# Kernel tuning notes

Measured on AMD Instinct MI355X. Metric: run time of the kernel, lower is better.

The kernel has to match this reference:

```python
import jax, jax.numpy as jnp
import numpy as np
import math

D, H = 128, 8
B, LC, LQ = 8, 512, 64


def pos_signal(channels, length):
    # tensor2tensor timing signal, returned as [C, L]
    pos = jnp.arange(length, dtype=jnp.float32)
    nts = channels // 2
    inc = math.log(1.0e4) / (nts - 1)
    inv = jnp.exp(jnp.arange(nts, dtype=jnp.float32) * -inc)
    st = pos[:, None] * inv[None, :]                      # [L, nts]
    sig = jnp.concatenate([jnp.sin(st), jnp.cos(st)], 1)  # [L, C]
    return sig.T


def mask_logits(t, m):
    return t * m + (1.0 - m) * -1e30


def ln_c(x, g, b):  # LayerNorm over channel dim of [B, D, L]
    mu = jnp.mean(x, axis=1, keepdims=True)
    var = jnp.mean((x - mu) ** 2, axis=1, keepdims=True)
    return (x - mu) / jnp.sqrt(var + 1e-5) * g[None, :, None] + b[None, :, None]


def conv1x1(x, w, b=None):  # x [B, I, L], w [O, I]
    y = jnp.einsum('oi,bil->bol', w, x)
    return y if b is None else y + b[None, :, None]


def dw_sep_conv(x, dw, pw, pwb):  # depthwise (k, no bias) -> pointwise (bias) -> relu
    k = dw.shape[-1]
    y = jax.lax.conv_general_dilated(x, dw[:, None, :], (1,), [(k // 2, k // 2)],
        dimension_numbers=('NCH', 'OIH', 'NCH'), feature_group_count=x.shape[1])
    return jax.nn.relu(conv1x1(y, pw, pwb))


def self_attention(x, mem_w, q_w, mask, n_head):  # x [B, D, L]
    b, d, L = x.shape
    dh = d // n_head
    mem = jnp.einsum('oi,bil->blo', mem_w, x)  # [B, L, 2D]
    q = jnp.einsum('oi,bil->blo', q_w, x)      # [B, L, D]
    def heads(t):
        return t.reshape(b, L, n_head, dh).transpose(0, 2, 1, 3)  # [B, H, L, dh]
    Qh = heads(q) * dh ** -0.5
    K = heads(mem[..., :d])
    V = heads(mem[..., d:])
    logits = jnp.einsum('bhqe,bhke->bhqk', Qh, K)
    logits = mask_logits(logits, mask[:, None, None, :])
    w = jax.nn.softmax(logits, axis=-1)
    o = jnp.einsum('bhqk,bhke->bhqe', w, V)
    return o.transpose(0, 2, 1, 3).reshape(b, L, d).transpose(0, 2, 1)


def encoder_block(x, mask, p, n_head):
    out = x + pos_signal(x.shape[1], x.shape[2])[None]
    n_conv = p['dw'].shape[0]
    for i in range(n_conv):
        res = out
        out = ln_c(out, p['lnc_g'][i], p['lnc_b'][i])
        out = dw_sep_conv(out, p['dw'][i], p['pw'][i], p['pw_b'][i]) + res
    res = out
    out = ln_c(out, p['ln1_g'], p['ln1_b'])
    out = self_attention(out, p['mem_w'], p['q_w'], mask, n_head) + res
    res = out
    out = ln_c(out, p['ln2_g'], p['ln2_b'])
    out = jax.nn.relu(conv1x1(out, p['ffn1_w'], p['ffn1_b']))
    out = conv1x1(out, p['ffn2_w'], p['ffn2_b'])
    return out + res


def cq_attention(Ce, Qe, cmask, qmask, w4C, w4Q, w4mlu, cq_b):
    Cx = Ce.transpose(0, 2, 1)   # [B, Lc, 2D]
    Qx = Qe.transpose(0, 2, 1)   # [B, Lq, 2D]
    s0 = jnp.einsum('bld,d->bl', Cx, w4C)[:, :, None]
    s1 = jnp.einsum('bqd,d->bq', Qx, w4Q)[:, None, :]
    s2 = jnp.einsum('bld,bqd->blq', Cx * w4mlu[None, None, :], Qx)
    S = s0 + s1 + s2 + cq_b
    S1 = jax.nn.softmax(mask_logits(S, qmask[:, None, :]), axis=2)
    S2 = jax.nn.softmax(mask_logits(S, cmask[:, :, None]), axis=1)
    A = jnp.einsum('blq,bqd->bld', S1, Qx)
    Bt = jnp.einsum('blq,bmq,bmd->bld', S1, S2, Cx)  # (S1 @ S2^T) @ C
    out = jnp.concatenate([Cx, A, Cx * A, Cx * Bt], axis=2)
    return out.transpose(0, 2, 1)  # [B, 8D, Lc]


def _forward(C, Q, maskC, maskQ, e_dw, e_pw, e_pw_b, e_lnc_g, e_lnc_b, e_mem_w, e_q_w,
             e_ffn1_w, e_ffn1_b, e_ffn2_w, e_ffn2_b, e_ln1_g, e_ln1_b, e_ln2_g, e_ln2_b,
             w4C, w4Q, w4mlu, cq_b, resizer_w,
             m_dw, m_pw, m_pw_b, m_lnc_g, m_lnc_b, m_mem_w, m_q_w,
             m_ffn1_w, m_ffn1_b, m_ffn2_w, m_ffn2_b, m_ln1_g, m_ln1_b, m_ln2_g, m_ln2_b):
    ep = dict(dw=e_dw, pw=e_pw, pw_b=e_pw_b, lnc_g=e_lnc_g, lnc_b=e_lnc_b,
              mem_w=e_mem_w, q_w=e_q_w, ffn1_w=e_ffn1_w, ffn1_b=e_ffn1_b,
              ffn2_w=e_ffn2_w, ffn2_b=e_ffn2_b, ln1_g=e_ln1_g, ln1_b=e_ln1_b,
              ln2_g=e_ln2_g, ln2_b=e_ln2_b)
    mp = dict(dw=m_dw, pw=m_pw, pw_b=m_pw_b, lnc_g=m_lnc_g, lnc_b=m_lnc_b,
              mem_w=m_mem_w, q_w=m_q_w, ffn1_w=m_ffn1_w, ffn1_b=m_ffn1_b,
              ffn2_w=m_ffn2_w, ffn2_b=m_ffn2_b, ln1_g=m_ln1_g, ln1_b=m_ln1_b,
              ln2_g=m_ln2_g, ln2_b=m_ln2_b)
    Ce = encoder_block(C, maskC, ep, H)
    Qe = encoder_block(Q, maskQ, ep, H)
    Ce = jnp.concatenate([Ce, C], axis=1)  # encode_fusion -> [B, 2D, Lc]
    Qe = jnp.concatenate([Qe, Q], axis=1)
    X = cq_attention(Ce, Qe, maskC, maskQ, w4C, w4Q, w4mlu, cq_b)
    X = jnp.concatenate([X, Ce], axis=1)   # match_fusion -> [B, 10D, Lc]
    M0 = conv1x1(X, resizer_w)             # [B, D, Lc]

    def run(m):
        def step(carry, p):
            return encoder_block(carry, maskC, p, H), None
        m, _ = jax.lax.scan(step, m, mp)
        return m

    M1 = run(M0)
    M2 = run(M1)
    M3 = run(M2)
    return M1, M2, M3


def setup_inputs() -> dict:
    key = jax.random.key(0)
    ks = iter(jax.random.split(key, 48))
    def rn(shape, scale):
        return jax.random.normal(next(ks), shape, dtype=jnp.float32) * scale
    s1 = 1.0 / math.sqrt(D)
    s2 = 1.0 / math.sqrt(2 * D)
    f32 = jnp.float32
    return dict(
        C=rn((B, D, LC), 1.0), Q=rn((B, D, LQ), 1.0),
        maskC=jnp.ones((B, LC), f32), maskQ=jnp.ones((B, LQ), f32),
        e_dw=rn((4, D, 7), 1.0 / math.sqrt(7)), e_pw=rn((4, D, D), s1),
        e_pw_b=jnp.zeros((4, D), f32), e_lnc_g=jnp.ones((4, D), f32), e_lnc_b=jnp.zeros((4, D), f32),
        e_mem_w=rn((2 * D, D), s1), e_q_w=rn((D, D), s1),
        e_ffn1_w=rn((D, D), s1), e_ffn1_b=jnp.zeros((D,), f32),
        e_ffn2_w=rn((D, D), s1), e_ffn2_b=jnp.zeros((D,), f32),
        e_ln1_g=jnp.ones((D,), f32), e_ln1_b=jnp.zeros((D,), f32),
        e_ln2_g=jnp.ones((D,), f32), e_ln2_b=jnp.zeros((D,), f32),
        w4C=rn((2 * D,), s2), w4Q=rn((2 * D,), s2), w4mlu=rn((2 * D,), s2),
        cq_b=jnp.zeros((1,), f32),
        resizer_w=rn((D, 10 * D), 1.0 / math.sqrt(10 * D)),
        m_dw=rn((7, 2, D, 5), 1.0 / math.sqrt(5)), m_pw=rn((7, 2, D, D), s1),
        m_pw_b=jnp.zeros((7, 2, D), f32), m_lnc_g=jnp.ones((7, 2, D), f32), m_lnc_b=jnp.zeros((7, 2, D), f32),
        m_mem_w=rn((7, 2 * D, D), s1), m_q_w=rn((7, D, D), s1),
        m_ffn1_w=rn((7, D, D), s1), m_ffn1_b=jnp.zeros((7, D), f32),
        m_ffn2_w=rn((7, D, D), s1), m_ffn2_b=jnp.zeros((7, D), f32),
        m_ln1_g=jnp.ones((7, D), f32), m_ln1_b=jnp.zeros((7, D), f32),
        m_ln2_g=jnp.ones((7, D), f32), m_ln2_b=jnp.zeros((7, D), f32),
    )


def reference(C, Q, maskC, maskQ, e_dw, e_pw, e_pw_b, e_lnc_g, e_lnc_b, e_mem_w, e_q_w,
              e_ffn1_w, e_ffn1_b, e_ffn2_w, e_ffn2_b, e_ln1_g, e_ln1_b, e_ln2_g, e_ln2_b,
              w4C, w4Q, w4mlu, cq_b, resizer_w,
              m_dw, m_pw, m_pw_b, m_lnc_g, m_lnc_b, m_mem_w, m_q_w,
              m_ffn1_w, m_ffn1_b, m_ffn2_w, m_ffn2_b, m_ln1_g, m_ln1_b, m_ln2_g, m_ln2_b):
    return _forward(C, Q, maskC, maskQ, e_dw, e_pw, e_pw_b, e_lnc_g, e_lnc_b, e_mem_w, e_q_w,
                    e_ffn1_w, e_ffn1_b, e_ffn2_w, e_ffn2_b, e_ln1_g, e_ln1_b, e_ln2_g, e_ln2_b,
                    w4C, w4Q, w4mlu, cq_b, resizer_w,
                    m_dw, m_pw, m_pw_b, m_lnc_g, m_lnc_b, m_mem_w, m_q_w,
                    m_ffn1_w, m_ffn1_b, m_ffn2_w, m_ffn2_b, m_ln1_g, m_ln1_b, m_ln2_g, m_ln2_b)
```

## Files before the change

kernel.cpp:

```cpp
#include <hip/hip_runtime.h>
#include <math.h>

#define D_  128
#define B_  8
#define H_  8
#define LC_ 512
#define LQ_ 64

typedef float f32x4 __attribute__((ext_vector_type(4)));
typedef short bf16x8 __attribute__((ext_vector_type(8)));
typedef short short4v __attribute__((ext_vector_type(4)));
typedef unsigned short ushortT;

__device__ inline short bfr(float x) {
  unsigned u = __float_as_uint(x);
  u += 0x7fff + ((u >> 16) & 1);
  return (short)(u >> 16);
}
__device__ inline float bfi(ushortT u) {
  return __uint_as_float(((unsigned)u) << 16);
}

__device__ inline bf16x8 mk8(short4v lo, short4v hi) {
  bf16x8 r;
  r[0] = lo[0]; r[1] = lo[1]; r[2] = lo[2]; r[3] = lo[3];
  r[4] = hi[0]; r[5] = hi[1]; r[6] = hi[2]; r[7] = hi[3];
  return r;
}

__device__ inline bf16x8 ldA(const ushortT* row, int koff) {
  short4v lo = *(const short4v*)(row + koff);
  short4v hi = *(const short4v*)(row + koff + 16);
  return mk8(lo, hi);
}
__device__ inline bf16x8 ldB2(const ushortT* plo, const ushortT* phi) {
  short4v lo = *(const short4v*)plo;
  short4v hi = *(const short4v*)phi;
  return mk8(lo, hi);
}

__global__ void k_prep(const float* a0, const float* a1, const float* a2,
                       const float* a3, const float* a4, const float* a5,
                       const float* a6, const float* a7, const float* a8,
                       const float* a9, const float* a10, ushortT* dst) {
  int i = blockIdx.x * 256 + threadIdx.x;
  if (i >= 1114112) return;
  const float* s; int lo;
  if      (i <   65536) { s = a0;  lo = i; }
  else if (i <   98304) { s = a1;  lo = i - 65536; }
  else if (i <  114688) { s = a2;  lo = i - 98304; }
  else if (i <  131072) { s = a3;  lo = i - 114688; }
  else if (i <  147456) { s = a4;  lo = i - 131072; }
  else if (i <  311296) { s = a5;  lo = i - 147456; }
  else if (i <  540672) { s = a6;  lo = i - 311296; }
  else if (i <  770048) { s = a7;  lo = i - 540672; }
  else if (i <  884736) { s = a8;  lo = i - 770048; }
  else if (i <  999424) { s = a9;  lo = i - 884736; }
  else                  { s = a10; lo = i - 999424; }
  dst[i] = (ushortT)bfr(s[lo]);
}

template <int KK, int ADDPOS>
__global__ __launch_bounds__(256) void k_fusedconv(
    const float* __restrict__ x, float* __restrict__ yout,
    const float* __restrict__ dw1, const ushortT* __restrict__ pw1,
    const float* __restrict__ pb1, const float* __restrict__ g1,
    const float* __restrict__ be1,
    const float* __restrict__ dw2, const ushortT* __restrict__ pw2,
    const float* __restrict__ pb2, const float* __restrict__ g2w,
    const float* __restrict__ be2, int L) {
  const int HALO = KK / 2;
  const int W1 = 32 + 2 * HALO;
  __shared__ __align__(16) float raw[128 * 40];
  __shared__ __align__(16) ushortT l1o[128 * 36];
  __shared__ __align__(16) ushortT xbf1[32 * 32 * 4];
  __shared__ float mu1[40], rs1[40], mu2[32], rs2[32], ps[160], psq[160];
  ushortT* xbf2 = (ushortT*)raw;
  int l0 = blockIdx.x * 16;
  int o0 = blockIdx.y * 64;
  int b = blockIdx.z;
  int tid = threadIdx.x;
  for (int idx = tid; idx < 128 * W1; idx += 256) {
    int d = idx / W1, c = idx - d * W1;
    int gl = l0 - 8 - HALO + c;
    float v = 0.f;
    if (gl >= 0 && gl < L) {
      v = x[((size_t)b * 128 + d) * L + gl];
      if (ADDPOS) {
        int j = d & 63;
        float arg = (float)gl * expf(-(float)j * 0.14619588f);
        v += (d < 64) ? sinf(arg) : cosf(arg);
      }
    }
    raw[d * 40 + c] = v;
  }
  __syncthreads();
  if (tid < 4 * W1) {
    int c = tid % W1, hh = tid / W1;
    float s = 0.f, s2 = 0.f;
    for (int d = hh * 32; d < hh * 32 + 32; d++) {
      float v = raw[d * 40 + c];
      s += v; s2 += v * v;
    }
    ps[tid] = s; psq[tid] = s2;
  }
  __syncthreads();
  if (tid < W1) {
    float s = ps[tid] + ps[tid + W1] + ps[tid + 2 * W1] + ps[tid + 3 * W1];
    float s2 = psq[tid] + psq[tid + W1] + psq[tid + 2 * W1] + psq[tid + 3 * W1];
    float mu = s * (1.f / 128.f);
    float var = fmaxf(s2 * (1.f / 128.f) - mu * mu, 0.f);
    mu1[tid] = mu; rs1[tid] = rsqrtf(var + 1e-5f);
  }
  __syncthreads();
  {
    int cc0 = tid & 31, dbase = tid >> 5;
#pragma unroll
    for (int kq = 0; kq < 4; kq++) {
      short4v pk;
#pragma unroll
      for (int e = 0; e < 4; e++) {
        int d = dbase * 16 + kq * 4 + e;
        float gg = g1[d], bb = be1[d];
        const float* wr = dw1 + d * KK;
        float acc = 0.f;
#pragma unroll
        for (int t = 0; t < KK; t++) {
          int ci = cc0 + t;
          int gl = l0 - 8 - HALO + ci;
          float lv = 0.f;
          if (gl >= 0 && gl < L)
            lv = (raw[d * 40 + ci] - mu1[ci]) * rs1[ci] * gg + bb;
          acc += wr[t] * lv;
        }
        pk[e] = bfr(acc);
      }
      *(short4v*)&xbf1[(((dbase * 4 + kq) * 32) + cc0) * 4] = pk;
    }
  }
  __syncthreads();
  int w = tid >> 6, lane = tid & 63, g2 = lane >> 4, r = lane & 15;
  {
    f32x4 acc[2][2];
#pragma unroll
    for (int i = 0; i < 2; i++)
#pragma unroll
      for (int nt = 0; nt < 2; nt++) acc[i][nt] = (f32x4){0.f, 0.f, 0.f, 0.f};
#pragma unroll
    for (int i = 0; i < 2; i++) {
      const ushortT* arow = pw1 + (size_t)((2 * w + i) * 16 + r) * 128;
#pragma unroll
      for (int kk = 0; kk < 4; kk++) {
        bf16x8 a = ldA(arow, kk * 32 + g2 * 4);
#pragma unroll
        for (int nt = 0; nt < 2; nt++) {
          bf16x8 bb = ldB2(&xbf1[(((kk * 8 + g2) * 32) + nt * 16 + r) * 4],
                           &xbf1[(((kk * 8 + 4 + g2) * 32) + nt * 16 + r) * 4]);
          acc[i][nt] = __builtin_amdgcn_mfma_f32_16x16x32_bf16(a, bb, acc[i][nt], 0, 0, 0);
        }
      }
    }
#pragma unroll
    for (int i = 0; i < 2; i++)
#pragma unroll
      for (int nt = 0; nt < 2; nt++)
#pragma unroll
        for (int p = 0; p < 4; p++) {
          int o = (2 * w + i) * 16 + g2 * 4 + p;
          int c1 = nt * 16 + r;
          int gl = l0 - 8 + c1;
          float val = 0.f;
          if (gl >= 0 && gl < L)
            val = fmaxf(acc[i][nt][p] + pb1[o], 0.f) + raw[o * 40 + c1 + HALO];
          l1o[o * 36 + c1] = (ushortT)bfr(val);
        }
  }
  __syncthreads();
  if (tid < 128) {
    int c = tid & 31, hh = tid >> 5;
    float s = 0.f, s2 = 0.f;
    for (int d = hh * 32; d < hh * 32 + 32; d++) {
      float v = bfi(l1o[d * 36 + c]);
      s += v; s2 += v * v;
    }
    ps[tid] = s; psq[tid] = s2;
  }
  __syncthreads();
  if (tid < 32) {
    float s = ps[tid] + ps[tid + 32] + ps[tid + 64] + ps[tid + 96];
    float s2 = psq[tid] + psq[tid + 32] + psq[tid + 64] + psq[tid + 96];
    float mu = s * (1.f / 128.f);
    float var = fmaxf(s2 * (1.f / 128.f) - mu * mu, 0.f);
    mu2[tid] = mu; rs2[tid] = rsqrtf(var + 1e-5f);
  }
  __syncthreads();
  {
    int cc2 = tid & 15, db2 = tid >> 4;
#pragma unroll
    for (int kq = 0; kq < 2; kq++) {
      short4v pk;
#pragma unroll
      for (int e = 0; e < 4; e++) {
        int d = db2 * 8 + kq * 4 + e;
        float gg = g2w[d], bb = be2[d];
        const float* wr = dw2 + d * KK;
        float acc = 0.f;
#pragma unroll
        for (int t = 0; t < KK; t++) {
          int c1 = cc2 + 8 + t - HALO;
          int gl = l0 + cc2 + t - HALO;
          float lv = 0.f;
          if (gl >= 0 && gl < L)
            lv = (bfi(l1o[d * 36 + c1]) - mu2[c1]) * rs2[c1] * gg + bb;
          acc += wr[t] * lv;
        }
        pk[e] = bfr(acc);
      }
      *(short4v*)&xbf2[(((db2 * 2 + kq) * 16) + cc2) * 4] = pk;
    }
  }
  __syncthreads();
  {
    f32x4 a2 = {0.f, 0.f, 0.f, 0.f};
    const ushortT* arow = pw2 + (size_t)(o0 + 16 * w + r) * 128;
#pragma unroll
    for (int kk = 0; kk < 4; kk++) {
      bf16x8 a = ldA(arow, kk * 32 + g2 * 4);
      bf16x8 bb = ldB2(&xbf2[(((kk * 8 + g2) * 16) + r) * 4],
                       &xbf2[(((kk * 8 + 4 + g2) * 16) + r) * 4]);
      a2 = __builtin_amdgcn_mfma_f32_16x16x32_bf16(a, bb, a2, 0, 0, 0);
    }
#pragma unroll
    for (int p = 0; p < 4; p++) {
      int o = o0 + 16 * w + g2 * 4 + p;
      yout[((size_t)b * 128 + o) * L + l0 + r] =
          fmaxf(a2[p] + pb2[o], 0.f) + bfi(l1o[o * 36 + 8 + r]);
    }
  }
}

template <int KK, int ADDPOS>
__global__ __launch_bounds__(512) void k_convproj(
    const float* __restrict__ x, float* __restrict__ yout,
    const float* __restrict__ dw1, const ushortT* __restrict__ pw1,
    const float* __restrict__ pb1, const float* __restrict__ g1,
    const float* __restrict__ be1,
    const float* __restrict__ dw2, const ushortT* __restrict__ pw2,
    const float* __restrict__ pb2, const float* __restrict__ g2w,
    const float* __restrict__ be2,
    const ushortT* __restrict__ memw, const ushortT* __restrict__ qw,
    const float* __restrict__ g3, const float* __restrict__ be3,
    float* __restrict__ mkv, float* __restrict__ qp, int L) {
  const int HALO = KK / 2;
  const int W1 = 32 + 2 * HALO;
  __shared__ __align__(16) float raw[128 * 40];
  __shared__ __align__(16) ushortT l1o[128 * 36];
  __shared__ __align__(16) ushortT xbf1[32 * 32 * 4];
  __shared__ __align__(16) ushortT c2o[128 * 16];
  __shared__ float mu1[40], rs1[40], mu2[32], rs2[32], mu3[16], rs3[16];
  __shared__ float ps[512], psq[512];
  ushortT* xbf2 = (ushortT*)raw;
  ushortT* xbf3 = (ushortT*)(raw + 4096);
  int l0 = blockIdx.x * 16;
  int b = blockIdx.z;
  int tid = threadIdx.x;
  for (int idx = tid; idx < 128 * W1; idx += 512) {
    int d = idx / W1, c = idx - d * W1;
    int gl = l0 - 8 - HALO + c;
    float v = 0.f;
    if (gl >= 0 && gl < L) {
      v = x[((size_t)b * 128 + d) * L + gl];
      if (ADDPOS) {
        int j = d & 63;
        float arg = (float)gl * expf(-(float)j * 0.14619588f);
        v += (d < 64) ? sinf(arg) : cosf(arg);
      }
    }
    raw[d * 40 + c] = v;
  }
  __syncthreads();
  if (tid < 4 * W1) {
    int c = tid % W1, hh = tid / W1;
    float s = 0.f, s2 = 0.f;
    for (int d = hh * 32; d < hh * 32 + 32; d++) {
      float v = raw[d * 40 + c];
      s += v; s2 += v * v;
    }
    ps[tid] = s; psq[tid] = s2;
  }
  __syncthreads();
  if (tid < W1) {
    float s = ps[tid] + ps[tid + W1] + ps[tid + 2 * W1] + ps[tid + 3 * W1];
    float s2 = psq[tid] + psq[tid + W1] + psq[tid + 2 * W1] + psq[tid + 3 * W1];
    float mu = s * (1.f / 128.f);
    float var = fmaxf(s2 * (1.f / 128.f) - mu * mu, 0.f);
    mu1[tid] = mu; rs1[tid] = rsqrtf(var + 1e-5f);
  }
  __syncthreads();
  {
    int cc0 = tid & 31, dbase = tid >> 5;
#pragma unroll
    for (int kq = 0; kq < 2; kq++) {
      short4v pk;
#pragma unroll
      for (int e = 0; e < 4; e++) {
        int d = dbase * 8 + kq * 4 + e;
        float gg = g1[d], bb = be1[d];
        const float* wr = dw1 + d * KK;
        float acc = 0.f;
#pragma unroll
        for (int t = 0; t < KK; t++) {
          int ci = cc0 + t;
          int gl = l0 - 8 - HALO + ci;
          float lv = 0.f;
          if (gl >= 0 && gl < L)
            lv = (raw[d * 40 + ci] - mu1[ci]) * rs1[ci] * gg + bb;
          acc += wr[t] * lv;
        }
        pk[e] = bfr(acc);
      }
      *(short4v*)&xbf1[(((dbase * 2 + kq) * 32) + cc0) * 4] = pk;
    }
  }
  __syncthreads();
  int w = tid >> 6, lane = tid & 63, g2 = lane >> 4, r = lane & 15;
  {
    f32x4 acc[2];
    acc[0] = (f32x4){0.f, 0.f, 0.f, 0.f};
    acc[1] = (f32x4){0.f, 0.f, 0.f, 0.f};
    const ushortT* arow = pw1 + (size_t)(w * 16 + r) * 128;
#pragma unroll
    for (int kk = 0; kk < 4; kk++) {
      bf16x8 a = ldA(arow, kk * 32 + g2 * 4);
#pragma unroll
      for (int nt = 0; nt < 2; nt++) {
        bf16x8 bb = ldB2(&xbf1[(((kk * 8 + g2) * 32) + nt * 16 + r) * 4],
                         &xbf1[(((kk * 8 + 4 + g2) * 32) + nt * 16 + r) * 4]);
        acc[nt] = __builtin_amdgcn_mfma_f32_16x16x32_bf16(a, bb, acc[nt], 0, 0, 0);
      }
    }
#pragma unroll
    for (int nt = 0; nt < 2; nt++)
#pragma unroll
      for (int p = 0; p < 4; p++) {
        int o = w * 16 + g2 * 4 + p;
        int c1 = nt * 16 + r;
        int gl = l0 - 8 + c1;
        float val = 0.f;
        if (gl >= 0 && gl < L)
          val = fmaxf(acc[nt][p] + pb1[o], 0.f) + raw[o * 40 + c1 + HALO];
        l1o[o * 36 + c1] = (ushortT)bfr(val);
      }
  }
  __syncthreads();
  if (tid < 128) {
    int c = tid & 31, hh = tid >> 5;
    float s = 0.f, s2 = 0.f;
    for (int d = hh * 32; d < hh * 32 + 32; d++) {
      float v = bfi(l1o[d * 36 + c]);
      s += v; s2 += v * v;
    }
    ps[tid] = s; psq[tid] = s2;
  }
  __syncthreads();
  if (tid < 32) {
    float s = ps[tid] + ps[tid + 32] + ps[tid + 64] + ps[tid + 96];
    float s2 = psq[tid] + psq[tid + 32] + psq[tid + 64] + psq[tid + 96];
    float mu = s * (1.f / 128.f);
    float var = fmaxf(s2 * (1.f / 128.f) - mu * mu, 0.f);
    mu2[tid] = mu; rs2[tid] = rsqrtf(var + 1e-5f);
  }
  __syncthreads();
  {
    int cc2 = tid & 15, db2 = tid >> 4;
    short4v pk;
#pragma unroll
    for (int e = 0; e < 4; e++) {
      int d = db2 * 4 + e;
      float gg = g2w[d], bb = be2[d];
      const float* wr = dw2 + d * KK;
      float acc = 0.f;
#pragma unroll
      for (int t = 0; t < KK; t++) {
        int c1 = cc2 + 8 + t - HALO;
        int gl = l0 + cc2 + t - HALO;
        float lv = 0.f;
        if (gl >= 0 && gl < L)
          lv = (bfi(l1o[d * 36 + c1]) - mu2[c1]) * rs2[c1] * gg + bb;
        acc += wr[t] * lv;
      }
      pk[e] = bfr(acc);
    }
    *(short4v*)&xbf2[((db2 * 16) + cc2) * 4] = pk;
  }
  __syncthreads();
  {
    f32x4 a2 = {0.f, 0.f, 0.f, 0.f};
    const ushortT* arow = pw2 + (size_t)(w * 16 + r) * 128;
#pragma unroll
    for (int kk = 0; kk < 4; kk++) {
      bf16x8 a = ldA(arow, kk * 32 + g2 * 4);
      bf16x8 bb = ldB2(&xbf2[(((kk * 8 + g2) * 16) + r) * 4],
                       &xbf2[(((kk * 8 + 4 + g2) * 16) + r) * 4]);
      a2 = __builtin_amdgcn_mfma_f32_16x16x32_bf16(a, bb, a2, 0, 0, 0);
    }
#pragma unroll
    for (int p = 0; p < 4; p++) {
      int o = w * 16 + g2 * 4 + p;
      float val = fmaxf(a2[p] + pb2[o], 0.f) + bfi(l1o[o * 36 + 8 + r]);
      yout[((size_t)b * 128 + o) * L + l0 + r] = val;
      c2o[o * 16 + r] = (ushortT)bfr(val);
    }
  }
  __syncthreads();
  if (tid < 128) {
    int c = tid & 15, hh = tid >> 4;
    float s = 0.f, s2 = 0.f;
    for (int d = hh * 16; d < hh * 16 + 16; d++) {
      float v = bfi(c2o[d * 16 + c]);
      s += v; s2 += v * v;
    }
    ps[tid] = s; psq[tid] = s2;
  }
  __syncthreads();
  if (tid < 16) {
    float s = 0.f, s2 = 0.f;
#pragma unroll
    for (int hh = 0; hh < 8; hh++) { s += ps[hh * 16 + tid]; s2 += psq[hh * 16 + tid]; }
    float mu = s * (1.f / 128.f);
    float var = fmaxf(s2 * (1.f / 128.f) - mu * mu, 0.f);
    mu3[tid] = mu; rs3[tid] = rsqrtf(var + 1e-5f);
  }
  __syncthreads();
  for (int idx = tid; idx < 2048; idx += 512) {
    int d = idx >> 4, c = idx & 15;
    float val = (bfi(c2o[d * 16 + c]) - mu3[c]) * rs3[c] * g3[d] + be3[d];
    xbf3[(((d >> 2) * 16) + c) * 4 + (d & 3)] = (ushortT)bfr(val);
  }
  __syncthreads();
#pragma unroll
  for (int t = 0; t < 3; t++) {
    int mt = w + 8 * t;
    const ushortT* arow; float* outp; int obase, O;
    if (mt < 16) { arow = memw + (size_t)(mt * 16 + r) * 128; outp = mkv; obase = mt * 16; O = 256; }
    else         { arow = qw + (size_t)((mt - 16) * 16 + r) * 128; outp = qp; obase = (mt - 16) * 16; O = 128; }
    f32x4 acc = {0.f, 0.f, 0.f, 0.f};
#pragma unroll
    for (int kk = 0; kk < 4; kk++) {
      bf16x8 a = ldA(arow, kk * 32 + g2 * 4);
      bf16x8 bb = ldB2(&xbf3[(((kk * 8 + g2) * 16) + r) * 4],
                       &xbf3[(((kk * 8 + 4 + g2) * 16) + r) * 4]);
      acc = __builtin_amdgcn_mfma_f32_16x16x32_bf16(a, bb, acc, 0, 0, 0);
    }
#pragma unroll
    for (int p = 0; p < 4; p++)
      outp[((size_t)b * O + obase + g2 * 4 + p) * L + l0 + r] = acc[p];
  }
}

template <int NCH>
__global__ __launch_bounds__(1024) void k_attnffn(
    const float* __restrict__ memKV, const float* __restrict__ qp,
    const float* __restrict__ mask, float* __restrict__ cur,
    const ushortT* __restrict__ w1bf, const float* __restrict__ b1,
    const ushortT* __restrict__ w2bf, const float* __restrict__ b2,
    const float* __restrict__ g, const float* __restrict__ be, int L) {
  __shared__ float msh[8][64], ssh[8][64], Osh[8][64][4];
  __shared__ float updT[128 * 16];
  __shared__ __align__(16) ushortT xbf[32 * 16 * 4];
  __shared__ __align__(16) ushortT midbf[32 * 16 * 4];
  __shared__ float mu_s[16], rs_s[16], ps[1024], psq[1024];
  int q0 = blockIdx.x * 16;
  int b = blockIdx.z;
  int tid = threadIdx.x;
  int w = tid >> 6;
  int h = w & 7, kh = w >> 3;
  int lane = tid & 63;
  int g2 = lane >> 4, r = lane & 15;
  const float* qb = qp + ((size_t)b * 128 + h * 16) * L;
  const float* kb = memKV + ((size_t)b * 256 + h * 16) * L;
  const float* vb = memKV + ((size_t)b * 256 + 128 + h * 16) * L;
  const float* mk = mask + (size_t)b * L;
  int qcol = q0 + r;
  bf16x8 qf;
#pragma unroll
  for (int j = 0; j < 4; j++)
    qf[j] = bfr(qb[(size_t)(g2 * 4 + j) * L + qcol] * 0.25f);
  qf[4] = 0; qf[5] = 0; qf[6] = 0; qf[7] = 0;
  float m_run = -INFINITY, ssum = 0.f;
  f32x4 O = {0.f, 0.f, 0.f, 0.f};
  int kbeg = kh * (L / 2), kend = (kh + 1) * (L / 2);
  for (int k0 = kbeg; k0 < kend; k0 += NCH * 16) {
    f32x4 sd[NCH];
#pragma unroll
    for (int mc = 0; mc < NCH; mc++) {
      bf16x8 kf;
      int krow = k0 + mc * 16 + r;
#pragma unroll
      for (int j = 0; j < 4; j++)
        kf[j] = bfr(kb[(size_t)(g2 * 4 + j) * L + krow]);
      kf[4] = 0; kf[5] = 0; kf[6] = 0; kf[7] = 0;
      f32x4 z = {0.f, 0.f, 0.f, 0.f};
      sd[mc] = __builtin_amdgcn_mfma_f32_16x16x32_bf16(kf, qf, z, 0, 0, 0);
    }
    float tm = -INFINITY;
#pragma unroll
    for (int mc = 0; mc < NCH; mc++) {
#pragma unroll
      for (int p = 0; p < 4; p++) {
        float mv = mk[k0 + mc * 16 + g2 * 4 + p];
        float sv = sd[mc][p] * mv + (1.f - mv) * (-1e30f);
        sd[mc][p] = sv;
        tm = fmaxf(tm, sv);
      }
    }
    tm = fmaxf(tm, __shfl_xor(tm, 16));
    tm = fmaxf(tm, __shfl_xor(tm, 32));
    float nm = fmaxf(m_run, tm);
    float c = __expf(m_run - nm);
    ssum *= c;
    O[0] *= c; O[1] *= c; O[2] *= c; O[3] *= c;
    float psum = 0.f;
    bf16x8 pf[NCH / 2];
#pragma unroll
    for (int c2 = 0; c2 < NCH / 2; c2++) {
#pragma unroll
      for (int j = 0; j < 4; j++) {
        float e0 = __expf(sd[2 * c2][j] - nm);
        float e1 = __expf(sd[2 * c2 + 1][j] - nm);
        psum += e0 + e1;
        pf[c2][j] = bfr(e0);
        pf[c2][j + 4] = bfr(e1);
      }
    }
    psum += __shfl_xor(psum, 16);
    psum += __shfl_xor(psum, 32);
    ssum += psum;
#pragma unroll
    for (int c2 = 0; c2 < NCH / 2; c2++) {
      const float* vrow = vb + (size_t)r * L + k0 + c2 * 32 + g2 * 4;
      float4 v0 = *(const float4*)vrow;
      float4 v1 = *(const float4*)(vrow + 16);
      bf16x8 vf;
      vf[0] = bfr(v0.x); vf[1] = bfr(v0.y); vf[2] = bfr(v0.z); vf[3] = bfr(v0.w);
      vf[4] = bfr(v1.x); vf[5] = bfr(v1.y); vf[6] = bfr(v1.z); vf[7] = bfr(v1.w);
      O = __builtin_amdgcn_mfma_f32_16x16x32_bf16(vf, pf[c2], O, 0, 0, 0);
    }
    m_run = nm;
  }
  if (kh == 1) {
    msh[h][lane] = m_run;
    ssh[h][lane] = ssum;
#pragma unroll
    for (int p = 0; p < 4; p++) Osh[h][lane][p] = O[p];
  }
  __syncthreads();
  if (kh == 0) {
    float mB = msh[h][lane], sB = ssh[h][lane];
    float nm = fmaxf(m_run, mB);
    float cA = __expf(m_run - nm), cB = __expf(mB - nm);
    float inv = 1.f / (ssum * cA + sB * cB);
#pragma unroll
    for (int p = 0; p < 4; p++) {
      int d = h * 16 + g2 * 4 + p;
      float ov = (O[p] * cA + Osh[h][lane][p] * cB) * inv;
      updT[d * 16 + r] = cur[((size_t)b * 128 + d) * L + qcol] + ov;
    }
  }
  __syncthreads();
  {
    int c = tid & 15, hh = tid >> 4;
    float s = 0.f, s2 = 0.f;
    for (int d = hh * 2; d < hh * 2 + 2; d++) {
      float v = updT[d * 16 + c];
      s += v; s2 += v * v;
    }
    ps[tid] = s; psq[tid] = s2;
  }
  __syncthreads();
  if (tid < 16) {
    float s = 0.f, s2 = 0.f;
    for (int hh = 0; hh < 64; hh++) { s += ps[hh * 16 + tid]; s2 += psq[hh * 16 + tid]; }
    float mu = s * (1.f / 128.f);
    float var = fmaxf(s2 * (1.f / 128.f) - mu * mu, 0.f);
    mu_s[tid] = mu; rs_s[tid] = rsqrtf(var + 1e-5f);
  }
  __syncthreads();
  for (int idx = tid; idx < 2048; idx += 1024) {
    int d = idx >> 4, c = idx & 15;
    float val = (updT[d * 16 + c] - mu_s[c]) * rs_s[c] * g[d] + be[d];
    xbf[(((d >> 2) * 16) + c) * 4 + (d & 3)] = (ushortT)bfr(val);
  }
  __syncthreads();
  if (w < 8) {
    f32x4 acc = {0.f, 0.f, 0.f, 0.f};
    const ushortT* ar = w1bf + (size_t)(16 * w + r) * 128;
#pragma unroll
    for (int kk = 0; kk < 4; kk++) {
      bf16x8 a = ldA(ar, kk * 32 + g2 * 4);
      bf16x8 bb = ldB2(&xbf[(((kk * 8 + g2) * 16) + r) * 4],
                       &xbf[(((kk * 8 + 4 + g2) * 16) + r) * 4]);
      acc = __builtin_amdgcn_mfma_f32_16x16x32_bf16(a, bb, acc, 0, 0, 0);
    }
#pragma unroll
    for (int p = 0; p < 4; p++) {
      int dmid = 16 * w + g2 * 4 + p;
      float val = fmaxf(acc[p] + b1[dmid], 0.f);
      midbf[(((4 * w + g2) * 16) + r) * 4 + p] = (ushortT)bfr(val);
    }
  }
  __syncthreads();
  if (w < 8) {
    f32x4 a2 = {0.f, 0.f, 0.f, 0.f};
    const ushortT* ar = w2bf + (size_t)(16 * w + r) * 128;
#pragma unroll
    for (int kk = 0; kk < 4; kk++) {
      bf16x8 a = ldA(ar, kk * 32 + g2 * 4);
      bf16x8 bb = ldB2(&midbf[(((kk * 8 + g2) * 16) + r) * 4],
                       &midbf[(((kk * 8 + 4 + g2) * 16) + r) * 4]);
      a2 = __builtin_amdgcn_mfma_f32_16x16x32_bf16(a, bb, a2, 0, 0, 0);
    }
#pragma unroll
    for (int p = 0; p < 4; p++) {
      int o = 16 * w + g2 * 4 + p;
      cur[((size_t)b * 128 + o) * L + q0 + r] = a2[p] + b2[o] + updT[o * 16 + r];
    }
  }
}


__global__ void k_concat2(const float* __restrict__ x1, const float* __restrict__ x2,
                          float* __restrict__ out, int L, int total) {
  int idx = blockIdx.x * 256 + threadIdx.x;
  if (idx >= total) return;
  int l = idx % L;
  int c = (idx / L) & 255;
  int b = idx / (L * 256);
  float v = (c < 128) ? x1[((size_t)b * 128 + c) * L + l]
                      : x2[((size_t)b * 128 + (c - 128)) * L + l];
  out[idx] = v;
}

__global__ void k_cqSrow(const float* __restrict__ Ce, const float* __restrict__ Qe,
                         const float* __restrict__ w4C, const float* __restrict__ w4Q,
                         const float* __restrict__ w4mlu, const float* __restrict__ cqb,
                         const float* __restrict__ qmask,
                         float* __restrict__ S, float* __restrict__ S1) {
  int idx = blockIdx.x * 256 + threadIdx.x;
  int q = idx & 63;
  int l = (idx >> 6) % LC_;
  int b = (idx >> 6) / LC_;
  const float* ce = Ce + (size_t)b * 256 * LC_ + l;
  const float* qe = Qe + (size_t)b * 256 * LQ_ + q;
  float acc = 0.f, a0 = 0.f, a1 = 0.f;
#pragma unroll 8
  for (int j = 0; j < 256; j++) {
    float cv = ce[(size_t)j * LC_];
    float qv = qe[(size_t)j * LQ_];
    acc += cv * w4mlu[j] * qv;
    a0 += cv * w4C[j];
    a1 += qv * w4Q[j];
  }
  float sv = acc + a0 + a1 + cqb[0];
  S[idx] = sv;
  float mv = qmask[b * LQ_ + q];
  float v = sv * mv + (1.f - mv) * (-1e30f);
  float mx = v;
  for (int off = 32; off; off >>= 1) mx = fmaxf(mx, __shfl_xor(mx, off));
  float p = expf(v - mx);
  float s = p;
  for (int off = 32; off; off >>= 1) s += __shfl_xor(s, off);
  S1[idx] = p / s;
}

__global__ __launch_bounds__(256) void k_softmax_col(
    const float* __restrict__ S, const float* __restrict__ cmask, float* __restrict__ S2) {
  int q = blockIdx.x & 63, b = blockIdx.x >> 6;
  int tid = threadIdx.x;
  __shared__ float redm[4], reds[4];
  const float* col = S + (size_t)b * LC_ * LQ_ + q;
  const float* mk = cmask + b * LC_;
  float vm[2];
#pragma unroll
  for (int k = 0; k < 2; k++) {
    int l = tid + 256 * k;
    float mv = mk[l];
    vm[k] = col[(size_t)l * LQ_] * mv + (1.f - mv) * (-1e30f);
  }
  float mx = fmaxf(vm[0], vm[1]);
  for (int off = 32; off; off >>= 1) mx = fmaxf(mx, __shfl_xor(mx, off));
  if ((tid & 63) == 0) redm[tid >> 6] = mx;
  __syncthreads();
  mx = fmaxf(fmaxf(redm[0], redm[1]), fmaxf(redm[2], redm[3]));
  float e0 = expf(vm[0] - mx), e1 = expf(vm[1] - mx);
  float s = e0 + e1;
  for (int off = 32; off; off >>= 1) s += __shfl_xor(s, off);
  if ((tid & 63) == 0) reds[tid >> 6] = s;
  __syncthreads();
  float invs = 1.f / (reds[0] + reds[1] + reds[2] + reds[3]);
  float* out = S2 + (size_t)b * LC_ * LQ_ + q;
  out[(size_t)tid * LQ_] = e0 * invs;
  out[(size_t)(tid + 256) * LQ_] = e1 * invs;
}

__global__ void k_cqY(const float* __restrict__ S2, const float* __restrict__ Ce,
                      float* __restrict__ Y) {
  int idx = blockIdx.x * 256 + threadIdx.x;
  if (idx >= B_ * 256 * LQ_) return;
  int q = idx & 63;
  int j = (idx >> 6) & 255;
  int b = idx >> 14;
  const float* s2 = S2 + (size_t)b * LC_ * LQ_ + q;
  const float* ce = Ce + ((size_t)b * 256 + j) * LC_;
  float acc = 0.f;
#pragma unroll 8
  for (int l = 0; l < LC_; l++) acc += s2[(size_t)l * LQ_] * ce[l];
  Y[idx] = acc;
}

__global__ __launch_bounds__(256) void k_cqAB(
    const float* __restrict__ S1, const float* __restrict__ Qe, const float* __restrict__ Y,
    float* __restrict__ A, float* __restrict__ Bt) {
  __shared__ float s1s[64][65];
  int l0 = blockIdx.x * 64;
  int b = blockIdx.z;
  int tid = threadIdx.x;
  for (int idx = tid; idx < 64 * 64; idx += 256) {
    int l = idx >> 6, q = idx & 63;
    s1s[l][q] = S1[((size_t)b * LC_ + l0 + l) * LQ_ + q];
  }
  __syncthreads();
  int ll = tid & 63, jj = tid >> 6;
  int j = blockIdx.y * 4 + jj;
  const float* qe = Qe + ((size_t)b * 256 + j) * LQ_;
  const float* yb = Y + ((size_t)b * 256 + j) * LQ_;
  float a = 0.f, bt = 0.f;
#pragma unroll 8
  for (int q = 0; q < 64; q++) {
    float sv = s1s[ll][q];
    a += sv * qe[q];
    bt += sv * yb[q];
  }
  A[((size_t)b * 256 + j) * LC_ + l0 + ll] = a;
  Bt[((size_t)b * 256 + j) * LC_ + l0 + ll] = bt;
}

__global__ __launch_bounds__(256) void k_resizer_mfma(
    const float* __restrict__ Ce, const float* __restrict__ A,
    const float* __restrict__ Bt, const ushortT* __restrict__ wbf,
    float* __restrict__ y) {
  __shared__ __align__(16) ushortT xbf[16 * 16 * 4];
  int l0 = blockIdx.x * 16;
  int o0 = blockIdx.y * 64;
  int b = blockIdx.z;
  int tid = threadIdx.x;
  int w = tid >> 6, lane = tid & 63, g2 = lane >> 4, r = lane & 15;
  const ushortT* arow = wbf + (size_t)(o0 + 16 * w + r) * 1280;
  f32x4 acc0 = {0.f, 0.f, 0.f, 0.f};
  for (int kt = 0; kt < 1280; kt += 64) {
    __syncthreads();
    for (int idx = tid; idx < 1024; idx += 256) {
      int kloc = idx >> 4, cc = idx & 15;
      int ch = kt + kloc;
      int seg = ch >> 8;
      int j = ch & 255;
      size_t p = ((size_t)b * 256 + j) * LC_ + l0 + cc;
      float v;
      if (seg == 0 || seg == 4) v = Ce[p];
      else if (seg == 1) v = A[p];
      else if (seg == 2) v = Ce[p] * A[p];
      else v = Ce[p] * Bt[p];
      xbf[(((kloc >> 2) * 16) + cc) * 4 + (kloc & 3)] = (ushortT)bfr(v);
    }
    __syncthreads();
#pragma unroll
    for (int kk2 = 0; kk2 < 2; kk2++) {
      bf16x8 a = ldA(arow, kt + kk2 * 32 + g2 * 4);
      bf16x8 b0 = ldB2(&xbf[(((kk2 * 8 + g2) * 16) + r) * 4],
                       &xbf[(((kk2 * 8 + 4 + g2) * 16) + r) * 4]);
      acc0 = __builtin_amdgcn_mfma_f32_16x16x32_bf16(a, b0, acc0, 0, 0, 0);
    }
  }
#pragma unroll
  for (int p = 0; p < 4; p++) {
    int o = o0 + 16 * w + g2 * 4 + p;
    y[((size_t)b * D_ + o) * LC_ + l0 + r] = acc0[p];
  }
}


struct BlkP {
  int k;
  const float* lnc_g[4]; const float* lnc_b[4];
  const float* dw[4]; const ushortT* pw[4]; const float* pw_b[4];
  const ushortT* mem_w; const ushortT* q_w;
  const float* ln1_g; const float* ln1_b;
  const ushortT* ffn1_w; const float* ffn1_b;
  const ushortT* ffn2_w; const float* ffn2_b;
  const float* ln2_g; const float* ln2_b;
};

static void conv_pair_only(hipStream_t st, const float* in, float* out, int L,
                           const BlkP& P, int i0, bool addpos) {
  dim3 gc(L / 16, 2, B_);
  if (addpos)
    k_fusedconv<7, 1><<<gc, 256, 0, st>>>(in, out,
        P.dw[i0], P.pw[i0], P.pw_b[i0], P.lnc_g[i0], P.lnc_b[i0],
        P.dw[i0+1], P.pw[i0+1], P.pw_b[i0+1], P.lnc_g[i0+1], P.lnc_b[i0+1], L);
  else
    k_fusedconv<7, 0><<<gc, 256, 0, st>>>(in, out,
        P.dw[i0], P.pw[i0], P.pw_b[i0], P.lnc_g[i0], P.lnc_b[i0],
        P.dw[i0+1], P.pw[i0+1], P.pw_b[i0+1], P.lnc_g[i0+1], P.lnc_b[i0+1], L);
}

template <int KK, int ADDPOS>
static void convproj(hipStream_t st, const float* in, float* out, float* mkv,
                     float* qpb, int L, const BlkP& P, int i0) {
  k_convproj<KK, ADDPOS><<<dim3(L / 16, 1, B_), 512, 0, st>>>(in, out,
      P.dw[i0], P.pw[i0], P.pw_b[i0], P.lnc_g[i0], P.lnc_b[i0],
      P.dw[i0+1], P.pw[i0+1], P.pw_b[i0+1], P.lnc_g[i0+1], P.lnc_b[i0+1],
      P.mem_w, P.q_w, P.ln1_g, P.ln1_b, mkv, qpb, L);
}

static void attnffn(hipStream_t st, float* cur, float* mkv, float* qpb,
                    const float* mask, int L, const BlkP& P) {
  if (L == LC_)
    k_attnffn<8><<<dim3(L / 16, 1, B_), 1024, 0, st>>>(mkv, qpb, mask, cur,
        P.ffn1_w, P.ffn1_b, P.ffn2_w, P.ffn2_b, P.ln2_g, P.ln2_b, L);
  else
    k_attnffn<2><<<dim3(L / 16, 1, B_), 1024, 0, st>>>(mkv, qpb, mask, cur,
        P.ffn1_w, P.ffn1_b, P.ffn2_w, P.ffn2_b, P.ln2_g, P.ln2_b, L);
}

extern "C" void kernel_launch(void* const* d_in, const int* in_sizes, int n_in,
                              void* d_out, int out_size, void* d_ws, size_t ws_size,
                              hipStream_t stream) {
  (void)in_sizes; (void)n_in; (void)out_size; (void)ws_size;
  const float* C        = (const float*)d_in[0];
  const float* Q        = (const float*)d_in[1];
  const float* maskC    = (const float*)d_in[2];
  const float* maskQ    = (const float*)d_in[3];
  const float* e_dw     = (const float*)d_in[4];
  const float* e_pw     = (const float*)d_in[5];
  const float* e_pw_b   = (const float*)d_in[6];
  const float* e_lnc_g  = (const float*)d_in[7];
  const float* e_lnc_b  = (const float*)d_in[8];
  const float* e_mem_w  = (const float*)d_in[9];
  const float* e_q_w    = (const float*)d_in[10];
  const float* e_ffn1_w = (const float*)d_in[11];
  const float* e_ffn1_b = (const float*)d_in[12];
  const float* e_ffn2_w = (const float*)d_in[13];
  const float* e_ffn2_b = (const float*)d_in[14];
  const float* e_ln1_g  = (const float*)d_in[15];
  const float* e_ln1_b  = (const float*)d_in[16];
  const float* e_ln2_g  = (const float*)d_in[17];
  const float* e_ln2_b  = (const float*)d_in[18];
  const float* w4C      = (const float*)d_in[19];
  const float* w4Q      = (const float*)d_in[20];
  const float* w4mlu    = (const float*)d_in[21];
  const float* cq_b     = (const float*)d_in[22];
  const float* resizer_w= (const float*)d_in[23];
  const float* m_dw     = (const float*)d_in[24];
  const float* m_pw     = (const float*)d_in[25];
  const float* m_pw_b   = (const float*)d_in[26];
  const float* m_lnc_g  = (const float*)d_in[27];
  const float* m_lnc_b  = (const float*)d_in[28];
  const float* m_mem_w  = (const float*)d_in[29];
  const float* m_q_w    = (const float*)d_in[30];
  const float* m_ffn1_w = (const float*)d_in[31];
  const float* m_ffn1_b = (const float*)d_in[32];
  const float* m_ffn2_w = (const float*)d_in[33];
  const float* m_ffn2_b = (const float*)d_in[34];
  const float* m_ln1_g  = (const float*)d_in[35];
  const float* m_ln1_b  = (const float*)d_in[36];
  const float* m_ln2_g  = (const float*)d_in[37];
  const float* m_ln2_b  = (const float*)d_in[38];

  float* ws = (float*)d_ws;
  const size_t SB = (size_t)B_ * D_ * LC_;
  float* cur  = ws;
  float* aux  = cur + SB;
  float* mkv  = aux + SB;
  float* qpb  = mkv + 2 * SB;
  float* Ce   = qpb + SB;
  float* Qe   = Ce + 2 * SB;
  float* Sbuf = Qe + (size_t)B_ * 256 * LQ_;
  float* S1   = Sbuf + (size_t)B_ * LC_ * LQ_;
  float* S2   = S1 + (size_t)B_ * LC_ * LQ_;
  float* Yb   = S2 + (size_t)B_ * LC_ * LQ_;
  float* Mb   = Yb + (size_t)B_ * 256 * LQ_;
  float* Ab   = mkv;
  float* Bb   = cur;
  ushortT* wb = (ushortT*)(Mb + SB);
  ushortT* w_epw  = wb;
  ushortT* w_emem = wb + 65536;
  ushortT* w_eq   = wb + 98304;
  ushortT* w_ef1  = wb + 114688;
  ushortT* w_ef2  = wb + 131072;
  ushortT* w_rsz  = wb + 147456;
  ushortT* w_mpw  = wb + 311296;
  ushortT* w_mmem = wb + 540672;
  ushortT* w_mq   = wb + 770048;
  ushortT* w_mf1  = wb + 884736;
  ushortT* w_mf2  = wb + 999424;

  k_prep<<<(1114112 + 255) / 256, 256, 0, stream>>>(
      e_pw, e_mem_w, e_q_w, e_ffn1_w, e_ffn2_w, resizer_w,
      m_pw, m_mem_w, m_q_w, m_ffn1_w, m_ffn2_w, wb);

  BlkP ep{};
  ep.k = 7;
  for (int i = 0; i < 4; i++) {
    ep.lnc_g[i] = e_lnc_g + i * 128;
    ep.lnc_b[i] = e_lnc_b + i * 128;
    ep.dw[i]    = e_dw + i * 128 * 7;
    ep.pw[i]    = w_epw + (size_t)i * 128 * 128;
    ep.pw_b[i]  = e_pw_b + i * 128;
  }
  ep.mem_w = w_emem; ep.q_w = w_eq;
  ep.ln1_g = e_ln1_g; ep.ln1_b = e_ln1_b;
  ep.ffn1_w = w_ef1; ep.ffn1_b = e_ffn1_b;
  ep.ffn2_w = w_ef2; ep.ffn2_b = e_ffn2_b;
  ep.ln2_g = e_ln2_g; ep.ln2_b = e_ln2_b;

  conv_pair_only(stream, C, cur, LC_, ep, 0, true);
  convproj<7, 0>(stream, cur, aux, mkv, qpb, LC_, ep, 2);
  attnffn(stream, aux, mkv, qpb, maskC, LC_, ep);
  {
    int tot = B_ * 256 * LC_;
    k_concat2<<<(tot + 255) / 256, 256, 0, stream>>>(aux, C, Ce, LC_, tot);
  }
  conv_pair_only(stream, Q, cur, LQ_, ep, 0, true);
  convproj<7, 0>(stream, cur, aux, mkv, qpb, LQ_, ep, 2);
  attnffn(stream, aux, mkv, qpb, maskQ, LQ_, ep);
  {
    int tot = B_ * 256 * LQ_;
    k_concat2<<<(tot + 255) / 256, 256, 0, stream>>>(aux, Q, Qe, LQ_, tot);
  }

  k_cqSrow<<<(B_ * LC_ * LQ_) / 256, 256, 0, stream>>>(Ce, Qe, w4C, w4Q, w4mlu, cq_b, maskQ, Sbuf, S1);
  k_softmax_col<<<B_ * LQ_, 256, 0, stream>>>(Sbuf, maskC, S2);
  k_cqY<<<(B_ * 256 * LQ_) / 256, 256, 0, stream>>>(S2, Ce, Yb);
  k_cqAB<<<dim3(LC_ / 64, 64, B_), 256, 0, stream>>>(S1, Qe, Yb, Ab, Bb);
  k_resizer_mfma<<<dim3(LC_ / 16, 2, B_), 256, 0, stream>>>(Ce, Ab, Bb, w_rsz, Mb);

  float* out = (float*)d_out;
  float* bufs[2] = {cur, aux};
  int cb = 0;
  const float* src = Mb;
  for (int r = 0; r < 3; r++) {
    for (int bi = 0; bi < 7; bi++) {
      BlkP mp{};
      mp.k = 5;
      for (int ci = 0; ci < 2; ci++) {
        int pc = bi * 2 + ci;
        mp.lnc_g[ci] = m_lnc_g + pc * 128;
        mp.lnc_b[ci] = m_lnc_b + pc * 128;
        mp.dw[ci]    = m_dw + pc * 128 * 5;
        mp.pw[ci]    = w_mpw + (size_t)pc * 128 * 128;
        mp.pw_b[ci]  = m_pw_b + pc * 128;
      }
      mp.mem_w  = w_mmem + (size_t)bi * 256 * 128;
      mp.q_w    = w_mq + (size_t)bi * 128 * 128;
      mp.ffn1_w = w_mf1 + (size_t)bi * 128 * 128;
      mp.ffn1_b = m_ffn1_b + bi * 128;
      mp.ffn2_w = w_mf2 + (size_t)bi * 128 * 128;
      mp.ffn2_b = m_ffn2_b + bi * 128;
      mp.ln1_g = m_ln1_g + bi * 128; mp.ln1_b = m_ln1_b + bi * 128;
      mp.ln2_g = m_ln2_g + bi * 128; mp.ln2_b = m_ln2_b + bi * 128;
      float* ob = bufs[cb];
      convproj<5, 1>(stream, src, ob, mkv, qpb, LC_, mp, 0);
      attnffn(stream, ob, mkv, qpb, maskC, LC_, mp);
      src = ob;
      cb ^= 1;
    }
    hipMemcpyAsync(out + (size_t)r * SB, src, SB * sizeof(float),
                   hipMemcpyDeviceToDevice, stream);
  }
}
```

Before: 1.441 ms.

## Run convproj with 1024 threads and write final block output directly

Grows the fused conv+projection kernel from 512 to 1024 threads per block and redistributes the depthwise conv, the first pointwise MFMA (one n-tile per wave), the second depthwise conv and the mem/q projection tiles across 16 waves. Separately, the last attention/FFN kernel of each model-encoder pass now also stores its result into the output buffer, which removes three device-to-device memcpys. The larger block adds parallelism per tile but leaves some waves idle in several phases and may lower occupancy or raise register pressure.

New measurement: 1.395 ms. 3.1% less time.

```diff
diff --git a/kernel.cpp b/kernel.cpp
--- a/kernel.cpp
+++ b/kernel.cpp
@@ -240,7 +240,7 @@
 }
 
 template <int KK, int ADDPOS>
-__global__ __launch_bounds__(512) void k_convproj(
+__global__ __launch_bounds__(1024) void k_convproj1024(
     const float* __restrict__ x, float* __restrict__ yout,
     const float* __restrict__ dw1, const ushortT* __restrict__ pw1,
     const float* __restrict__ pb1, const float* __restrict__ g1,
@@ -258,13 +258,13 @@
   __shared__ __align__(16) ushortT xbf1[32 * 32 * 4];
   __shared__ __align__(16) ushortT c2o[128 * 16];
   __shared__ float mu1[40], rs1[40], mu2[32], rs2[32], mu3[16], rs3[16];
-  __shared__ float ps[512], psq[512];
+  __shared__ float ps[160], psq[160];
   ushortT* xbf2 = (ushortT*)raw;
   ushortT* xbf3 = (ushortT*)(raw + 4096);
   int l0 = blockIdx.x * 16;
   int b = blockIdx.z;
   int tid = threadIdx.x;
-  for (int idx = tid; idx < 128 * W1; idx += 512) {
+  for (int idx = tid; idx < 128 * W1; idx += 1024) {
     int d = idx / W1, c = idx - d * W1;
     int gl = l0 - 8 - HALO + c;
     float v = 0.f;
@@ -299,58 +299,49 @@
   __syncthreads();
   {
     int cc0 = tid & 31, dbase = tid >> 5;
-#pragma unroll
-    for (int kq = 0; kq < 2; kq++) {
-      short4v pk;
-#pragma unroll
-      for (int e = 0; e < 4; e++) {
-        int d = dbase * 8 + kq * 4 + e;
-        float gg = g1[d], bb = be1[d];
-        const float* wr = dw1 + d * KK;
-        float acc = 0.f;
-#pragma unroll
-        for (int t = 0; t < KK; t++) {
-          int ci = cc0 + t;
-          int gl = l0 - 8 - HALO + ci;
-          float lv = 0.f;
-          if (gl >= 0 && gl < L)
-            lv = (raw[d * 40 + ci] - mu1[ci]) * rs1[ci] * gg + bb;
-          acc += wr[t] * lv;
-        }
-        pk[e] = bfr(acc);
-      }
-      *(short4v*)&xbf1[(((dbase * 2 + kq) * 32) + cc0) * 4] = pk;
-    }
+    short4v pk;
+#pragma unroll
+    for (int e = 0; e < 4; e++) {
+      int d = dbase * 4 + e;
+      float gg = g1[d], bb = be1[d];
+      const float* wr = dw1 + d * KK;
+      float acc = 0.f;
+#pragma unroll
+      for (int t = 0; t < KK; t++) {
+        int ci = cc0 + t;
+        int gl = l0 - 8 - HALO + ci;
+        float lv = 0.f;
+        if (gl >= 0 && gl < L)
+          lv = (raw[d * 40 + ci] - mu1[ci]) * rs1[ci] * gg + bb;
+        acc += wr[t] * lv;
+      }
+      pk[e] = bfr(acc);
+    }
+    *(short4v*)&xbf1[((dbase * 32) + cc0) * 4] = pk;
   }
   __syncthreads();
   int w = tid >> 6, lane = tid & 63, g2 = lane >> 4, r = lane & 15;
   {
-    f32x4 acc[2];
-    acc[0] = (f32x4){0.f, 0.f, 0.f, 0.f};
-    acc[1] = (f32x4){0.f, 0.f, 0.f, 0.f};
-    const ushortT* arow = pw1 + (size_t)(w * 16 + r) * 128;
+    int m = w & 7, nt = w >> 3;
+    f32x4 acc = {0.f, 0.f, 0.f, 0.f};
+    const ushortT* arow = pw1 + (size_t)(m * 16 + r) * 128;
 #pragma unroll
     for (int kk = 0; kk < 4; kk++) {
       bf16x8 a = ldA(arow, kk * 32 + g2 * 4);
-#pragma unroll
-      for (int nt = 0; nt < 2; nt++) {
-        bf16x8 bb = ldB2(&xbf1[(((kk * 8 + g2) * 32) + nt * 16 + r) * 4],
-                         &xbf1[(((kk * 8 + 4 + g2) * 32) + nt * 16 + r) * 4]);
-        acc[nt] = __builtin_amdgcn_mfma_f32_16x16x32_bf16(a, bb, acc[nt], 0, 0, 0);
-      }
-    }
-#pragma unroll
-    for (int nt = 0; nt < 2; nt++)
-#pragma unroll
-      for (int p = 0; p < 4; p++) {
-        int o = w * 16 + g2 * 4 + p;
-        int c1 = nt * 16 + r;
-        int gl = l0 - 8 + c1;
-        float val = 0.f;
-        if (gl >= 0 && gl < L)
-          val = fmaxf(acc[nt][p] + pb1[o], 0.f) + raw[o * 40 + c1 + HALO];
-        l1o[o * 36 + c1] = (ushortT)bfr(val);
-      }
+      bf16x8 bb = ldB2(&xbf1[(((kk * 8 + g2) * 32) + nt * 16 + r) * 4],
+                       &xbf1[(((kk * 8 + 4 + g2) * 32) + nt * 16 + r) * 4]);
+      acc = __builtin_amdgcn_mfma_f32_16x16x32_bf16(a, bb, acc, 0, 0, 0);
+    }
+#pragma unroll
+    for (int p = 0; p < 4; p++) {
+      int o = m * 16 + g2 * 4 + p;
+      int c1 = nt * 16 + r;
+      int gl = l0 - 8 + c1;
+      float val = 0.f;
+      if (gl >= 0 && gl < L)
+        val = fmaxf(acc[p] + pb1[o], 0.f) + raw[o * 40 + c1 + HALO];
+      l1o[o * 36 + c1] = (ushortT)bfr(val);
+    }
   }
   __syncthreads();
   if (tid < 128) {
@@ -373,10 +364,9 @@
   __syncthreads();
   {
     int cc2 = tid & 15, db2 = tid >> 4;
-    short4v pk;
-#pragma unroll
-    for (int e = 0; e < 4; e++) {
-      int d = db2 * 4 + e;
+#pragma unroll
+    for (int e = 0; e < 2; e++) {
+      int d = db2 * 2 + e;
       float gg = g2w[d], bb = be2[d];
       const float* wr = dw2 + d * KK;
       float acc = 0.f;
@@ -389,12 +379,11 @@
           lv = (bfi(l1o[d * 36 + c1]) - mu2[c1]) * rs2[c1] * gg + bb;
         acc += wr[t] * lv;
       }
-      pk[e] = bfr(acc);
-    }
-    *(short4v*)&xbf2[((db2 * 16) + cc2) * 4] = pk;
-  }
-  __syncthreads();
-  {
+      xbf2[(((d >> 2) * 16) + cc2) * 4 + (d & 3)] = (ushortT)bfr(acc);
+    }
+  }
+  __syncthreads();
+  if (w < 8) {
     f32x4 a2 = {0.f, 0.f, 0.f, 0.f};
     const ushortT* arow = pw2 + (size_t)(w * 16 + r) * 128;
 #pragma unroll
@@ -432,39 +421,42 @@
     mu3[tid] = mu; rs3[tid] = rsqrtf(var + 1e-5f);
   }
   __syncthreads();
-  for (int idx = tid; idx < 2048; idx += 512) {
+  for (int idx = tid; idx < 2048; idx += 1024) {
     int d = idx >> 4, c = idx & 15;
     float val = (bfi(c2o[d * 16 + c]) - mu3[c]) * rs3[c] * g3[d] + be3[d];
     xbf3[(((d >> 2) * 16) + c) * 4 + (d & 3)] = (ushortT)bfr(val);
   }
   __syncthreads();
 #pragma unroll
-  for (int t = 0; t < 3; t++) {
-    int mt = w + 8 * t;
-    const ushortT* arow; float* outp; int obase, O;
-    if (mt < 16) { arow = memw + (size_t)(mt * 16 + r) * 128; outp = mkv; obase = mt * 16; O = 256; }
-    else         { arow = qw + (size_t)((mt - 16) * 16 + r) * 128; outp = qp; obase = (mt - 16) * 16; O = 128; }
-    f32x4 acc = {0.f, 0.f, 0.f, 0.f};
-#pragma unroll
-    for (int kk = 0; kk < 4; kk++) {
-      bf16x8 a = ldA(arow, kk * 32 + g2 * 4);
-      bf16x8 bb = ldB2(&xbf3[(((kk * 8 + g2) * 16) + r) * 4],
-                       &xbf3[(((kk * 8 + 4 + g2) * 16) + r) * 4]);
-      acc = __builtin_amdgcn_mfma_f32_16x16x32_bf16(a, bb, acc, 0, 0, 0);
-    }
-#pragma unroll
-    for (int p = 0; p < 4; p++)
-      outp[((size_t)b * O + obase + g2 * 4 + p) * L + l0 + r] = acc[p];
-  }
-}
-
-template <int NCH>
+  for (int t = 0; t < 2; t++) {
+    int mt = w + 16 * t;
+    if (mt < 24) {
+      const ushortT* arow; float* outp; int obase, O;
+      if (mt < 16) { arow = memw + (size_t)(mt * 16 + r) * 128; outp = mkv; obase = mt * 16; O = 256; }
+      else         { arow = qw + (size_t)((mt - 16) * 16 + r) * 128; outp = qp; obase = (mt - 16) * 16; O = 128; }
+      f32x4 acc = {0.f, 0.f, 0.f, 0.f};
+#pragma unroll
+      for (int kk = 0; kk < 4; kk++) {
+        bf16x8 a = ldA(arow, kk * 32 + g2 * 4);
+        bf16x8 bb = ldB2(&xbf3[(((kk * 8 + g2) * 16) + r) * 4],
+                         &xbf3[(((kk * 8 + 4 + g2) * 16) + r) * 4]);
+        acc = __builtin_amdgcn_mfma_f32_16x16x32_bf16(a, bb, acc, 0, 0, 0);
+      }
+#pragma unroll
+      for (int p = 0; p < 4; p++)
+        outp[((size_t)b * O + obase + g2 * 4 + p) * L + l0 + r] = acc[p];
+    }
+  }
+}
+
+template <int NCH, int WOUT>
 __global__ __launch_bounds__(1024) void k_attnffn(
     const float* __restrict__ memKV, const float* __restrict__ qp,
     const float* __restrict__ mask, float* __restrict__ cur,
     const ushortT* __restrict__ w1bf, const float* __restrict__ b1,
     const ushortT* __restrict__ w2bf, const float* __restrict__ b2,
-    const float* __restrict__ g, const float* __restrict__ be, int L) {
+    const float* __restrict__ g, const float* __restrict__ be,
+    float* __restrict__ wout, int L) {
   __shared__ float msh[8][64], ssh[8][64], Osh[8][64][4];
   __shared__ float updT[128 * 16];
   __shared__ __align__(16) ushortT xbf[32 * 16 * 4];
@@ -623,7 +615,10 @@
 #pragma unroll
     for (int p = 0; p < 4; p++) {
       int o = 16 * w + g2 * 4 + p;
-      cur[((size_t)b * 128 + o) * L + q0 + r] = a2[p] + b2[o] + updT[o * 16 + r];
+      size_t pos = ((size_t)b * 128 + o) * L + q0 + r;
+      float val = a2[p] + b2[o] + updT[o * 16 + r];
+      cur[pos] = val;
+      if (WOUT) wout[pos] = val;
     }
   }
 }
@@ -816,20 +811,26 @@
 template <int KK, int ADDPOS>
 static void convproj(hipStream_t st, const float* in, float* out, float* mkv,
                      float* qpb, int L, const BlkP& P, int i0) {
-  k_convproj<KK, ADDPOS><<<dim3(L / 16, 1, B_), 512, 0, st>>>(in, out,
+  k_convproj1024<KK, ADDPOS><<<dim3(L / 16, 1, B_), 1024, 0, st>>>(in, out,
       P.dw[i0], P.pw[i0], P.pw_b[i0], P.lnc_g[i0], P.lnc_b[i0],
       P.dw[i0+1], P.pw[i0+1], P.pw_b[i0+1], P.lnc_g[i0+1], P.lnc_b[i0+1],
       P.mem_w, P.q_w, P.ln1_g, P.ln1_b, mkv, qpb, L);
 }
 
 static void attnffn(hipStream_t st, float* cur, float* mkv, float* qpb,
-                    const float* mask, int L, const BlkP& P) {
-  if (L == LC_)
-    k_attnffn<8><<<dim3(L / 16, 1, B_), 1024, 0, st>>>(mkv, qpb, mask, cur,
-        P.ffn1_w, P.ffn1_b, P.ffn2_w, P.ffn2_b, P.ln2_g, P.ln2_b, L);
-  else
-    k_attnffn<2><<<dim3(L / 16, 1, B_), 1024, 0, st>>>(mkv, qpb, mask, cur,
-        P.ffn1_w, P.ffn1_b, P.ffn2_w, P.ffn2_b, P.ln2_g, P.ln2_b, L);
+                    const float* mask, int L, const BlkP& P, float* wout) {
+  dim3 g(L / 16, 1, B_);
+  if (L == LC_) {
+    if (wout)
+      k_attnffn<8, 1><<<g, 1024, 0, st>>>(mkv, qpb, mask, cur,
+          P.ffn1_w, P.ffn1_b, P.ffn2_w, P.ffn2_b, P.ln2_g, P.ln2_b, wout, L);
+    else
+      k_attnffn<8, 0><<<g, 1024, 0, st>>>(mkv, qpb, mask, cur,
+          P.ffn1_w, P.ffn1_b, P.ffn2_w, P.ffn2_b, P.ln2_g, P.ln2_b, nullptr, L);
+  } else {
+    k_attnffn<2, 0><<<g, 1024, 0, st>>>(mkv, qpb, mask, cur,
+        P.ffn1_w, P.ffn1_b, P.ffn2_w, P.ffn2_b, P.ln2_g, P.ln2_b, nullptr, L);
+  }
 }
 
 extern "C" void kernel_launch(void* const* d_in, const int* in_sizes, int n_in,
@@ -925,14 +926,14 @@
 
   conv_pair_only(stream, C, cur, LC_, ep, 0, true);
   convproj<7, 0>(stream, cur, aux, mkv, qpb, LC_, ep, 2);
-  attnffn(stream, aux, mkv, qpb, maskC, LC_, ep);
+  attnffn(stream, aux, mkv, qpb, maskC, LC_, ep, nullptr);
   {
     int tot = B_ * 256 * LC_;
     k_concat2<<<(tot + 255) / 256, 256, 0, stream>>>(aux, C, Ce, LC_, tot);
   }
   conv_pair_only(stream, Q, cur, LQ_, ep, 0, true);
   convproj<7, 0>(stream, cur, aux, mkv, qpb, LQ_, ep, 2);
-  attnffn(stream, aux, mkv, qpb, maskQ, LQ_, ep);
+  attnffn(stream, aux, mkv, qpb, maskQ, LQ_, ep, nullptr);
   {
     int tot = B_ * 256 * LQ_;
     k_concat2<<<(tot + 255) / 256, 256, 0, stream>>>(aux, Q, Qe, LQ_, tot);
@@ -970,11 +971,10 @@
       mp.ln2_g = m_ln2_g + bi * 128; mp.ln2_b = m_ln2_b + bi * 128;
       float* ob = bufs[cb];
       convproj<5, 1>(stream, src, ob, mkv, qpb, LC_, mp, 0);
-      attnffn(stream, ob, mkv, qpb, maskC, LC_, mp);
+      float* wout = (bi == 6) ? out + (size_t)r * SB : nullptr;
+      attnffn(stream, ob, mkv, qpb, maskC, LC_, mp, wout);
       src = ob;
       cb ^= 1;
     }
-    hipMemcpyAsync(out + (size_t)r * SB, src, SB * sizeof(float),
-                   hipMemcpyDeviceToDevice, stream);
-  }
-}
+  }
+}
```
